# Optimization experiments

Measured on AMD Instinct MI355X. Metric: run time of the kernel, lower is better.

The kernel has to match this reference:

```python
import jax, jax.numpy as jnp
import numpy as np

D_MODEL = 1024
H = 16
D_K = D_MODEL // H

def setup_inputs() -> dict:
    key = jax.random.key(0)
    k1, k2, k3, k4, k5 = jax.random.split(key, 5)
    x = jax.random.normal(k1, (2, 2048, D_MODEL), dtype=jnp.float32)
    s = 1.0 / np.sqrt(D_MODEL)
    W_qkv = jax.random.uniform(k2, (D_MODEL, 3 * D_MODEL), jnp.float32, -s, s)
    b_qkv = jax.random.uniform(k3, (3 * D_MODEL,), jnp.float32, -s, s)
    W_o = jax.random.uniform(k4, (D_MODEL, D_MODEL), jnp.float32, -s, s)
    b_o = jax.random.uniform(k5, (D_MODEL,), jnp.float32, -s, s)
    return {"x": x, "W_qkv": W_qkv, "b_qkv": b_qkv, "W_o": W_o, "b_o": b_o}

def reference(x, W_qkv, b_qkv, W_o, b_o):
    B, L, _ = x.shape
    qkv = x @ W_qkv + b_qkv                      # [B, L, 3*d_model]
    q, k, v = jnp.split(qkv, 3, axis=-1)
    def split_heads(t):
        return t.reshape(B, L, H, D_K).transpose(0, 2, 1, 3)  # [B,H,L,D_k]
    q, k, v = split_heads(q), split_heads(k), split_heads(v)
    scores = jnp.einsum('bhqd,bhkd->bhqk', q, k) / np.sqrt(D_K).astype(jnp.float32)
    attn = jax.nn.softmax(scores, axis=-1)       # [B,H,L,L]
    ctx = jnp.einsum('bhqk,bhkd->bhqd', attn, v)
    ctx = ctx.transpose(0, 2, 1, 3).reshape(B, L, H * D_K)
    out = ctx @ W_o + b_o                        # dropout is identity at eval
    return (out, attn)
```

## Files before the change

### kernel.cpp

```cpp
#include <hip/hip_runtime.h>
#include <stdint.h>

typedef __attribute__((ext_vector_type(8))) short bf16x8;
typedef __attribute__((ext_vector_type(4))) float f32x4;
typedef __attribute__((ext_vector_type(4))) unsigned int u32x4;
typedef __attribute__((ext_vector_type(2))) unsigned int u32x2;
typedef __attribute__((ext_vector_type(4))) unsigned short u16x4;

#define DEVINL static __device__ __forceinline__

DEVINL unsigned short f2bf(float f) {
  uint32_t u = __builtin_bit_cast(uint32_t, f);
  u = (u + 0x7FFFu + ((u >> 16) & 1u)) >> 16;
  return (unsigned short)u;
}

DEVINL float fexp2(float x) {
#if __has_builtin(__builtin_amdgcn_exp2f)
  return __builtin_amdgcn_exp2f(x);
#else
  return __expf(x * 0.69314718056f);
#endif
}

DEVINL void raw_barrier() {
  __builtin_amdgcn_sched_barrier(0);
  __builtin_amdgcn_s_barrier();
  __builtin_amdgcn_sched_barrier(0);
}

DEVINL void barrier_lds_only() {
  asm volatile("s_waitcnt lgkmcnt(0)" ::: "memory");
  raw_barrier();
}

DEVINL void async16(const unsigned short* lds, const unsigned short* g) {
  __builtin_amdgcn_global_load_lds(
      (const __attribute__((address_space(1))) unsigned int*)g,
      (__attribute__((address_space(3))) unsigned int*)lds, 16, 0, 0);
}

__global__ __launch_bounds__(256) void k_prep(const float* __restrict__ x,
                                              unsigned short* __restrict__ xbf,
                                              const float* __restrict__ Wqkv,
                                              unsigned short* __restrict__ wqT,
                                              const float* __restrict__ Wo,
                                              unsigned short* __restrict__ woT) {
  int bid = blockIdx.x;
  int t = threadIdx.x;
  if (bid < 4096) {
    int i = bid * 256 + t;
    f32x4 v = *(const f32x4*)(x + (size_t)i * 4);
    u16x4 o;
    for (int j = 0; j < 4; ++j) o[j] = f2bf(v[j]);
    *(u16x4*)(xbf + (size_t)i * 4) = o;
    return;
  }
  __shared__ unsigned short tile[64][72];
  const float* in;
  unsigned short* out;
  int K = 1024, N, k0, n0;
  if (bid < 4864) {
    int b = bid - 4096;
    N = 3072; k0 = (b & 15) * 64; n0 = (b >> 4) * 64;
    in = Wqkv; out = wqT;
  } else {
    int b = bid - 4864;
    N = 1024; k0 = (b & 15) * 64; n0 = (b >> 4) * 64;
    in = Wo; out = woT;
  }
  int r = t >> 2, c0 = (t & 3) * 16;
  for (int j = 0; j < 4; ++j) {
    int col = c0 + j * 4;
    f32x4 v = *(const f32x4*)(in + (size_t)(k0 + r) * N + n0 + col);
    u16x4 o;
    for (int q = 0; q < 4; ++q) o[q] = f2bf(v[q]);
    *(u16x4*)(&tile[r][col]) = o;
  }
  __syncthreads();
  for (int j = 0; j < 4; ++j) {
    int kcol = c0 + j * 4;
    u16x4 o;
    for (int q = 0; q < 4; ++q) o[q] = tile[kcol + q][r];
    *(u16x4*)(out + (size_t)(n0 + r) * K + k0 + kcol) = o;
  }
}

template <int MODE>
__global__ __launch_bounds__(256) void k_gemm(const unsigned short* __restrict__ A,
                                              const unsigned short* __restrict__ Bt,
                                              const float* __restrict__ bias,
                                              unsigned short* __restrict__ Qb,
                                              unsigned short* __restrict__ Kb,
                                              unsigned short* __restrict__ Vt,
                                              float* __restrict__ outF) {
  constexpr int KD = 1024;
  __shared__ unsigned short sh[17408];
  unsigned short* lA = sh;
  unsigned short* lB = sh + 8192;
  int tid = threadIdx.x;
  int lane = tid & 63, w = tid >> 6;
  int wr = w >> 1, wc = w & 1;
  int m0 = blockIdx.x * 128, n0 = blockIdx.y * 128;
  int lr = lane & 15, lg = lane >> 4;

  f32x4 acc[4][4] = {};

  int srow = w * 32 + (lane >> 3);
  int scol = (lane & 7) * 8;
  const unsigned short* gA = A + (size_t)(m0 + srow) * KD + scol;
  const unsigned short* gB = Bt + (size_t)(n0 + srow) * KD + scol;

  for (int kk = 0; kk < KD; kk += 64) {
    for (int s = 0; s < 4; ++s) {
      async16(&lA[(w * 32 + s * 8) * 64], gA + (size_t)s * 8 * KD + kk);
      async16(&lB[(w * 32 + s * 8) * 64], gB + (size_t)s * 8 * KD + kk);
    }
    __syncthreads();
    for (int kq = 0; kq < 2; ++kq) {
      bf16x8 af[4], bfr[4];
      for (int i = 0; i < 4; ++i)
        af[i] = *(const bf16x8*)(&lA[(wr * 64 + i * 16 + lr) * 64 + (kq * 4 + lg) * 8]);
      for (int r = 0; r < 4; ++r)
        bfr[r] = *(const bf16x8*)(&lB[(wc * 64 + r * 16 + lr) * 64 + (kq * 4 + lg) * 8]);
      for (int i = 0; i < 4; ++i)
        for (int r = 0; r < 4; ++r)
          acc[i][r] = __builtin_amdgcn_mfma_f32_16x16x32_bf16(af[i], bfr[r], acc[i][r], 0, 0, 0);
    }
    __syncthreads();
  }

  if (MODE == 0) {
    int which = n0 >> 10;
    int head0 = (n0 & 1023) >> 6;
    int b_idx = m0 >> 11;
    int l0 = m0 & 2047;
    if (which < 2) {
      for (int r = 0; r < 4; ++r) {
        int nl = wc * 64 + r * 16 + lr;
        float bv = bias[n0 + nl];
        for (int i = 0; i < 4; ++i) {
          int mlb = wr * 64 + i * 16 + lg * 4;
          for (int jj = 0; jj < 4; ++jj)
            sh[(mlb + jj) * 136 + nl] = f2bf(acc[i][r][jj] + bv);
        }
      }
      __syncthreads();
      unsigned short* dst = (which == 0) ? Qb : Kb;
      for (int it = 0; it < 4; ++it) {
        int row = it * 64 + (tid >> 2);
        int ml = row & 127, hd = row >> 7;
        int c = (tid & 3) * 16;
        bf16x8 v0 = *(const bf16x8*)&sh[ml * 136 + hd * 64 + c];
        bf16x8 v1 = *(const bf16x8*)&sh[ml * 136 + hd * 64 + c + 8];
        size_t bh = (size_t)(b_idx * 16 + head0 + hd);
        size_t off = (bh * 2048 + l0 + ml) * 64 + c;
        *(bf16x8*)(dst + off) = v0;
        *(bf16x8*)(dst + off + 8) = v1;
      }
    } else {
      for (int r = 0; r < 4; ++r) {
        int nl = wc * 64 + r * 16 + lr;
        float bv = bias[n0 + nl];
        for (int i = 0; i < 4; ++i) {
          int mlb = wr * 64 + i * 16 + lg * 4;
          u16x4 pk;
          for (int jj = 0; jj < 4; ++jj) pk[jj] = f2bf(acc[i][r][jj] + bv);
          *(u16x4*)&sh[nl * 136 + mlb] = pk;
        }
      }
      __syncthreads();
      for (int it = 0; it < 4; ++it) {
        int nl = it * 32 + (tid >> 3);
        int c = (tid & 7) * 16;
        bf16x8 v0 = *(const bf16x8*)&sh[nl * 136 + c];
        bf16x8 v1 = *(const bf16x8*)&sh[nl * 136 + c + 8];
        int dk = nl & 63, hd = nl >> 6;
        size_t bh = (size_t)(b_idx * 16 + head0 + hd);
        size_t off = (bh * 64 + dk) * 2048 + l0 + c;
        *(bf16x8*)(Vt + off) = v0;
        *(bf16x8*)(Vt + off + 8) = v1;
      }
    }
  } else {
    for (int r = 0; r < 4; ++r) {
      int n = n0 + wc * 64 + r * 16 + lr;
      float bv = bias[n];
      for (int i = 0; i < 4; ++i) {
        int mb = m0 + wr * 64 + i * 16 + lg * 4;
        for (int jj = 0; jj < 4; ++jj)
          outF[(size_t)(mb + jj) * 1024 + n] = acc[i][r][jj] + bv;
      }
    }
  }
}

__global__ __launch_bounds__(256) void k_attn(const unsigned short* __restrict__ Qb,
                                              const unsigned short* __restrict__ Kb,
                                              const unsigned short* __restrict__ Vt,
                                              float* __restrict__ attn,
                                              unsigned short* __restrict__ ctx) {
  __shared__ unsigned short KVs[4][4096];
  __shared__ uint32_t Pb[4][32 * 36];
  int tid = threadIdx.x, lane = tid & 63, w = tid >> 6;
  int lr = lane & 15, lg = lane >> 4;
  int bid = blockIdx.x;
  int xcd = bid & 7, slot = bid >> 3;
  int bh = xcd * 4 + (slot >> 4);
  int qb = slot & 15;
  int q0 = qb * 128 + w * 32;
  int b_idx = bh >> 4, h = bh & 15;
  const unsigned short* Qh = Qb + (size_t)bh * 2048 * 64;
  const unsigned short* Kh = Kb + (size_t)bh * 2048 * 64;
  const unsigned short* Vh = Vt + (size_t)bh * 64 * 2048;
  uint32_t* PwB = &Pb[w][0];
  const float A2 = 0.125f * 1.44269504089f;
  int e7 = lr & 7;

  int srow = w * 8 + (lane >> 3);
  int sc = (lane & 7) ^ (srow & 7);
  const unsigned short* gK = Kh + (size_t)srow * 64 + sc * 8;
  const unsigned short* gV = Vh + (size_t)srow * 2048 + sc * 8;

  bf16x8 qf[2][2];
  for (int i = 0; i < 2; ++i)
    for (int kq = 0; kq < 2; ++kq)
      qf[i][kq] = *(const bf16x8*)(Qh + (size_t)(q0 + i * 16 + lr) * 64 + kq * 32 + lg * 8);

  float l_run[2] = {0.f, 0.f};

  async16(&KVs[0][(w * 8) * 64],       gK);
  async16(&KVs[0][((w + 4) * 8) * 64], gK + 2048);
  async16(&KVs[1][(w * 8) * 64],       gK + 4096);
  async16(&KVs[1][((w + 4) * 8) * 64], gK + 4096 + 2048);
  for (int kt = 0; kt < 32; ++kt) {
    const unsigned short* Kc = KVs[kt & 3];
    if (kt < 30) {
      async16(&KVs[(kt + 2) & 3][(w * 8) * 64],       gK + (size_t)(kt + 2) * 4096);
      async16(&KVs[(kt + 2) & 3][((w + 4) * 8) * 64], gK + (size_t)(kt + 2) * 4096 + 2048);
      asm volatile("s_waitcnt vmcnt(4)" ::: "memory");
    } else if (kt == 30) {
      asm volatile("s_waitcnt vmcnt(2)" ::: "memory");
    } else {
      asm volatile("s_waitcnt vmcnt(0)" ::: "memory");
    }
    raw_barrier();
    f32x4 acc[2][4] = {};
    for (int kq = 0; kq < 2; ++kq) {
      int j = kq * 4 + lg;
      bf16x8 kf[4];
      for (int r = 0; r < 4; ++r)
        kf[r] = *(const bf16x8*)&Kc[(r * 16 + lr) * 64 + ((j ^ e7) << 3)];
      for (int i = 0; i < 2; ++i)
        for (int r = 0; r < 4; ++r)
          acc[i][r] = __builtin_amdgcn_mfma_f32_16x16x32_bf16(kf[r], qf[i][kq], acc[i][r], 0, 0, 0);
    }
    for (int i = 0; i < 2; ++i)
      for (int r = 0; r < 4; ++r)
        l_run[i] += fexp2(acc[i][r][0] * A2) + fexp2(acc[i][r][1] * A2) +
                    fexp2(acc[i][r][2] * A2) + fexp2(acc[i][r][3] * A2);
  }
  float invl[2];
  for (int i = 0; i < 2; ++i) {
    float s = l_run[i];
    s += __shfl_xor(s, 16);
    s += __shfl_xor(s, 32);
    invl[i] = 1.0f / s;
  }

  f32x4 cacc[2][4] = {};
  float* attn_base = attn + (size_t)bh * 2048 * 2048;
  float* arow = attn_base + (size_t)(q0 + lg) * 2048 + lr * 4;

  barrier_lds_only();
  async16(&KVs[0][(w * 8) * 64],       gK);
  async16(&KVs[0][((w + 4) * 8) * 64], gK + 2048);
  async16(&KVs[2][(w * 8) * 64],       gV);
  async16(&KVs[2][((w + 4) * 8) * 64], gV + 65536);
  for (int kt = 0; kt < 32; ++kt) {
    int cur = kt & 1;
    if (kt < 31) {
      async16(&KVs[cur ^ 1][(w * 8) * 64],       gK + (size_t)(kt + 1) * 4096);
      async16(&KVs[cur ^ 1][((w + 4) * 8) * 64], gK + (size_t)(kt + 1) * 4096 + 2048);
      async16(&KVs[2 + (cur ^ 1)][(w * 8) * 64],       gV + (size_t)(kt + 1) * 64);
      async16(&KVs[2 + (cur ^ 1)][((w + 4) * 8) * 64], gV + (size_t)(kt + 1) * 64 + 65536);
    }
    if (kt == 0)       asm volatile("s_waitcnt vmcnt(4)" ::: "memory");
    else if (kt == 31) asm volatile("s_waitcnt vmcnt(8)" ::: "memory");
    else               asm volatile("s_waitcnt vmcnt(12)" ::: "memory");
    raw_barrier();
    const unsigned short* Kc = KVs[cur];
    const unsigned short* Vc = KVs[2 + cur];
    f32x4 acc[2][4] = {};
    for (int kq = 0; kq < 2; ++kq) {
      int j = kq * 4 + lg;
      bf16x8 kf[4];
      for (int r = 0; r < 4; ++r)
        kf[r] = *(const bf16x8*)&Kc[(r * 16 + lr) * 64 + ((j ^ e7) << 3)];
      for (int i = 0; i < 2; ++i)
        for (int r = 0; r < 4; ++r)
          acc[i][r] = __builtin_amdgcn_mfma_f32_16x16x32_bf16(kf[r], qf[i][kq], acc[i][r], 0, 0, 0);
    }
    for (int i = 0; i < 2; ++i)
      for (int r = 0; r < 4; ++r) {
        float p0 = fexp2(acc[i][r][0] * A2) * invl[i];
        float p1 = fexp2(acc[i][r][1] * A2) * invl[i];
        float p2 = fexp2(acc[i][r][2] * A2) * invl[i];
        float p3 = fexp2(acc[i][r][3] * A2) * invl[i];
        uint32_t u0, u1;
        asm("v_cvt_pk_bf16_f32 %0, %1, %2" : "=v"(u0) : "v"(p0), "v"(p1));
        asm("v_cvt_pk_bf16_f32 %0, %1, %2" : "=v"(u1) : "v"(p2), "v"(p3));
        u32x2 uu; uu[0] = u0; uu[1] = u1;
        *(u32x2*)&PwB[(i * 16 + lr) * 36 + r * 8 + lg * 2] = uu;
      }
    for (int s = 0; s < 8; ++s) {
      int row = s * 4 + lg;
      u32x2 d = *(const u32x2*)&PwB[row * 36 + lr * 2];
      f32x4 v;
      v[0] = __builtin_bit_cast(float, d[0] << 16);
      v[1] = __builtin_bit_cast(float, d[0] & 0xFFFF0000u);
      v[2] = __builtin_bit_cast(float, d[1] << 16);
      v[3] = __builtin_bit_cast(float, d[1] & 0xFFFF0000u);
      __builtin_nontemporal_store(v, (f32x4*)(arow + (size_t)s * 4 * 2048 + kt * 64));
    }
    for (int kq2 = 0; kq2 < 2; ++kq2) {
      int j = kq2 * 4 + lg;
      bf16x8 pa[2], vf[4];
      for (int i = 0; i < 2; ++i)
        pa[i] = *(const bf16x8*)&PwB[(i * 16 + lr) * 36 + kq2 * 16 + lg * 4];
      for (int nn = 0; nn < 4; ++nn)
        vf[nn] = *(const bf16x8*)&Vc[(nn * 16 + lr) * 64 + ((j ^ e7) << 3)];
      for (int i = 0; i < 2; ++i)
        for (int nn = 0; nn < 4; ++nn)
          cacc[i][nn] = __builtin_amdgcn_mfma_f32_16x16x32_bf16(pa[i], vf[nn], cacc[i][nn], 0, 0, 0);
    }
    barrier_lds_only();
  }

  for (int nn = 0; nn < 4; ++nn) {
    int d = nn * 16 + lr;
    for (int i = 0; i < 2; ++i)
      for (int jj = 0; jj < 4; ++jj) {
        int q = q0 + i * 16 + lg * 4 + jj;
        int tok = b_idx * 2048 + q;
        ctx[(size_t)tok * 1024 + h * 64 + d] = f2bf(cacc[i][nn][jj]);
      }
  }
}

extern "C" void kernel_launch(void* const* d_in, const int* in_sizes, int n_in,
                              void* d_out, int out_size, void* d_ws, size_t ws_size,
                              hipStream_t stream) {
  const float* x    = (const float*)d_in[0];
  const float* Wqkv = (const float*)d_in[1];
  const float* bqkv = (const float*)d_in[2];
  const float* Wo   = (const float*)d_in[3];
  const float* bo   = (const float*)d_in[4];
  float* out  = (float*)d_out;
  float* attn = out + (size_t)4096 * 1024;

  char* ws = (char*)d_ws;
  unsigned short* xbf = (unsigned short*)(ws);
  unsigned short* wqT = (unsigned short*)(ws + 8388608);
  unsigned short* woT = (unsigned short*)(ws + 14680064);
  unsigned short* Qb  = (unsigned short*)(ws + 16777216);
  unsigned short* Kb  = (unsigned short*)(ws + 25165824);
  unsigned short* Vt  = (unsigned short*)(ws + 33554432);
  unsigned short* ctx = (unsigned short*)(ws + 41943040);

  k_prep<<<dim3(5120), dim3(256), 0, stream>>>(x, xbf, Wqkv, wqT, Wo, woT);
  k_gemm<0><<<dim3(32, 24), dim3(256), 0, stream>>>(xbf, wqT, bqkv, Qb, Kb, Vt, nullptr);
  k_attn<<<dim3(512), dim3(256), 0, stream>>>(Qb, Kb, Vt, attn, ctx);
  k_gemm<1><<<dim3(32, 8), dim3(256), 0, stream>>>(ctx, woT, bo, nullptr, nullptr, nullptr, out);
}
```

Before: 222.7 us.

## Restructure attention K/V pipelining: one barrier per tile, paired K tiles, MFMA priority

The first-pass row-sum loop now processes two K tiles per barrier, issuing both prefetches after the barrier with a full vmcnt wait. The second pass moves its barrier to the top of the loop and drops the trailing barrier, leaving one barrier per iteration. The PV MFMA block now runs before the nontemporal attn stores, and MFMA sections are wrapped in s_setprio to favour matrix issue. The aim is fewer barriers and stores that overlap with compute, at the cost of shallower prefetch in the first pass and buffer-reuse timing that now depends on the top barrier for correctness.

```diff
diff --git a/kernel.cpp b/kernel.cpp
--- a/kernel.cpp
+++ b/kernel.cpp
@@ -27,11 +27,6 @@
   __builtin_amdgcn_sched_barrier(0);
   __builtin_amdgcn_s_barrier();
   __builtin_amdgcn_sched_barrier(0);
-}
-
-DEVINL void barrier_lds_only() {
-  asm volatile("s_waitcnt lgkmcnt(0)" ::: "memory");
-  raw_barrier();
 }
 
 DEVINL void async16(const unsigned short* lds, const unsigned short* g) {
@@ -233,32 +228,37 @@
   async16(&KVs[0][((w + 4) * 8) * 64], gK + 2048);
   async16(&KVs[1][(w * 8) * 64],       gK + 4096);
   async16(&KVs[1][((w + 4) * 8) * 64], gK + 4096 + 2048);
-  for (int kt = 0; kt < 32; ++kt) {
-    const unsigned short* Kc = KVs[kt & 3];
-    if (kt < 30) {
-      async16(&KVs[(kt + 2) & 3][(w * 8) * 64],       gK + (size_t)(kt + 2) * 4096);
-      async16(&KVs[(kt + 2) & 3][((w + 4) * 8) * 64], gK + (size_t)(kt + 2) * 4096 + 2048);
-      asm volatile("s_waitcnt vmcnt(4)" ::: "memory");
-    } else if (kt == 30) {
-      asm volatile("s_waitcnt vmcnt(2)" ::: "memory");
-    } else {
-      asm volatile("s_waitcnt vmcnt(0)" ::: "memory");
-    }
+  for (int j = 0; j < 16; ++j) {
+    asm volatile("s_waitcnt vmcnt(0) lgkmcnt(0)" ::: "memory");
     raw_barrier();
-    f32x4 acc[2][4] = {};
-    for (int kq = 0; kq < 2; ++kq) {
-      int j = kq * 4 + lg;
-      bf16x8 kf[4];
-      for (int r = 0; r < 4; ++r)
-        kf[r] = *(const bf16x8*)&Kc[(r * 16 + lr) * 64 + ((j ^ e7) << 3)];
+    if (j < 15) {
+      int t2 = 2 * j + 2, t3 = 2 * j + 3;
+      async16(&KVs[t2 & 3][(w * 8) * 64],       gK + (size_t)t2 * 4096);
+      async16(&KVs[t2 & 3][((w + 4) * 8) * 64], gK + (size_t)t2 * 4096 + 2048);
+      async16(&KVs[t3 & 3][(w * 8) * 64],       gK + (size_t)t3 * 4096);
+      async16(&KVs[t3 & 3][((w + 4) * 8) * 64], gK + (size_t)t3 * 4096 + 2048);
+    }
+    for (int u = 0; u < 2; ++u) {
+      int kt = 2 * j + u;
+      const unsigned short* Kc = KVs[kt & 3];
+      f32x4 acc[2][4] = {};
+      bf16x8 kf[2][4];
+      for (int kq = 0; kq < 2; ++kq) {
+        int jx = kq * 4 + lg;
+        for (int r = 0; r < 4; ++r)
+          kf[kq][r] = *(const bf16x8*)&Kc[(r * 16 + lr) * 64 + ((jx ^ e7) << 3)];
+      }
+      __builtin_amdgcn_s_setprio(1);
+      for (int kq = 0; kq < 2; ++kq)
+        for (int i = 0; i < 2; ++i)
+          for (int r = 0; r < 4; ++r)
+            acc[i][r] = __builtin_amdgcn_mfma_f32_16x16x32_bf16(kf[kq][r], qf[i][kq], acc[i][r], 0, 0, 0);
+      __builtin_amdgcn_s_setprio(0);
       for (int i = 0; i < 2; ++i)
         for (int r = 0; r < 4; ++r)
-          acc[i][r] = __builtin_amdgcn_mfma_f32_16x16x32_bf16(kf[r], qf[i][kq], acc[i][r], 0, 0, 0);
-    }
-    for (int i = 0; i < 2; ++i)
-      for (int r = 0; r < 4; ++r)
-        l_run[i] += fexp2(acc[i][r][0] * A2) + fexp2(acc[i][r][1] * A2) +
-                    fexp2(acc[i][r][2] * A2) + fexp2(acc[i][r][3] * A2);
+          l_run[i] += fexp2(acc[i][r][0] * A2) + fexp2(acc[i][r][1] * A2) +
+                      fexp2(acc[i][r][2] * A2) + fexp2(acc[i][r][3] * A2);
+    }
   }
   float invl[2];
   for (int i = 0; i < 2; ++i) {
@@ -272,35 +272,38 @@
   float* attn_base = attn + (size_t)bh * 2048 * 2048;
   float* arow = attn_base + (size_t)(q0 + lg) * 2048 + lr * 4;
 
-  barrier_lds_only();
+  asm volatile("s_waitcnt lgkmcnt(0)" ::: "memory");
+  raw_barrier();
   async16(&KVs[0][(w * 8) * 64],       gK);
   async16(&KVs[0][((w + 4) * 8) * 64], gK + 2048);
   async16(&KVs[2][(w * 8) * 64],       gV);
   async16(&KVs[2][((w + 4) * 8) * 64], gV + 65536);
   for (int kt = 0; kt < 32; ++kt) {
     int cur = kt & 1;
+    if (kt == 0) asm volatile("s_waitcnt vmcnt(0) lgkmcnt(0)" ::: "memory");
+    else         asm volatile("s_waitcnt vmcnt(8) lgkmcnt(0)" ::: "memory");
+    raw_barrier();
     if (kt < 31) {
       async16(&KVs[cur ^ 1][(w * 8) * 64],       gK + (size_t)(kt + 1) * 4096);
       async16(&KVs[cur ^ 1][((w + 4) * 8) * 64], gK + (size_t)(kt + 1) * 4096 + 2048);
       async16(&KVs[2 + (cur ^ 1)][(w * 8) * 64],       gV + (size_t)(kt + 1) * 64);
       async16(&KVs[2 + (cur ^ 1)][((w + 4) * 8) * 64], gV + (size_t)(kt + 1) * 64 + 65536);
     }
-    if (kt == 0)       asm volatile("s_waitcnt vmcnt(4)" ::: "memory");
-    else if (kt == 31) asm volatile("s_waitcnt vmcnt(8)" ::: "memory");
-    else               asm volatile("s_waitcnt vmcnt(12)" ::: "memory");
-    raw_barrier();
     const unsigned short* Kc = KVs[cur];
     const unsigned short* Vc = KVs[2 + cur];
     f32x4 acc[2][4] = {};
+    bf16x8 kf[2][4];
     for (int kq = 0; kq < 2; ++kq) {
-      int j = kq * 4 + lg;
-      bf16x8 kf[4];
+      int jx = kq * 4 + lg;
       for (int r = 0; r < 4; ++r)
-        kf[r] = *(const bf16x8*)&Kc[(r * 16 + lr) * 64 + ((j ^ e7) << 3)];
+        kf[kq][r] = *(const bf16x8*)&Kc[(r * 16 + lr) * 64 + ((jx ^ e7) << 3)];
+    }
+    __builtin_amdgcn_s_setprio(1);
+    for (int kq = 0; kq < 2; ++kq)
       for (int i = 0; i < 2; ++i)
         for (int r = 0; r < 4; ++r)
-          acc[i][r] = __builtin_amdgcn_mfma_f32_16x16x32_bf16(kf[r], qf[i][kq], acc[i][r], 0, 0, 0);
-    }
+          acc[i][r] = __builtin_amdgcn_mfma_f32_16x16x32_bf16(kf[kq][r], qf[i][kq], acc[i][r], 0, 0, 0);
+    __builtin_amdgcn_s_setprio(0);
     for (int i = 0; i < 2; ++i)
       for (int r = 0; r < 4; ++r) {
         float p0 = fexp2(acc[i][r][0] * A2) * invl[i];
@@ -313,6 +316,19 @@
         u32x2 uu; uu[0] = u0; uu[1] = u1;
         *(u32x2*)&PwB[(i * 16 + lr) * 36 + r * 8 + lg * 2] = uu;
       }
+    for (int kq2 = 0; kq2 < 2; ++kq2) {
+      int jx = kq2 * 4 + lg;
+      bf16x8 pa[2], vf[4];
+      for (int i = 0; i < 2; ++i)
+        pa[i] = *(const bf16x8*)&PwB[(i * 16 + lr) * 36 + kq2 * 16 + lg * 4];
+      for (int nn = 0; nn < 4; ++nn)
+        vf[nn] = *(const bf16x8*)&Vc[(nn * 16 + lr) * 64 + ((jx ^ e7) << 3)];
+      __builtin_amdgcn_s_setprio(1);
+      for (int i = 0; i < 2; ++i)
+        for (int nn = 0; nn < 4; ++nn)
+          cacc[i][nn] = __builtin_amdgcn_mfma_f32_16x16x32_bf16(pa[i], vf[nn], cacc[i][nn], 0, 0, 0);
+      __builtin_amdgcn_s_setprio(0);
+    }
     for (int s = 0; s < 8; ++s) {
       int row = s * 4 + lg;
       u32x2 d = *(const u32x2*)&PwB[row * 36 + lr * 2];
@@ -323,18 +339,6 @@
       v[3] = __builtin_bit_cast(float, d[1] & 0xFFFF0000u);
       __builtin_nontemporal_store(v, (f32x4*)(arow + (size_t)s * 4 * 2048 + kt * 64));
     }
-    for (int kq2 = 0; kq2 < 2; ++kq2) {
-      int j = kq2 * 4 + lg;
-      bf16x8 pa[2], vf[4];
-      for (int i = 0; i < 2; ++i)
-        pa[i] = *(const bf16x8*)&PwB[(i * 16 + lr) * 36 + kq2 * 16 + lg * 4];
-      for (int nn = 0; nn < 4; ++nn)
-        vf[nn] = *(const bf16x8*)&Vc[(nn * 16 + lr) * 64 + ((j ^ e7) << 3)];
-      for (int i = 0; i < 2; ++i)
-        for (int nn = 0; nn < 4; ++nn)
-          cacc[i][nn] = __builtin_amdgcn_mfma_f32_16x16x32_bf16(pa[i], vf[nn], cacc[i][nn], 0, 0, 0);
-    }
-    barrier_lds_only();
   }
 
   for (int nn = 0; nn < 4; ++nn) {
```

Result: faster. 217.0 us (-2.5%).
